# Optimization experiments

Hardware: AMD Instinct MI355X
Metric: run time of the kernel (lower is better)

The kernel has to match this reference:

```python
import jax, jax.numpy as jnp
import numpy as np

BATCH, SEQ, H, P, HID, CHUNK = 2, 2048, 32, 64, 2048, 256
NORM_EPS = 1e-5


def setup_inputs() -> dict:
    key = jax.random.key(0)
    ks = jax.random.split(key, 10)
    f = lambda k, sh, sc=1.0: jax.random.normal(k, sh, jnp.float32) * sc
    return {
        "hidden_states_ab": f(ks[0], (BATCH, SEQ, HID), 0.02),
        "hidden_states_g": f(ks[1], (BATCH, SEQ, HID), 0.02),
        "q_states": f(ks[2], (BATCH, SEQ, H, P)),
        "k_states": f(ks[3], (BATCH, SEQ, H, P)),
        "v_states": f(ks[4], (BATCH, SEQ, H, P)),
        "dt_w": f(ks[5], (HID, H), 0.02),
        "dt_b": jnp.zeros((H,), jnp.float32),
        "g_w": f(ks[6], (HID, H), 0.02),
        "g_b": jnp.zeros((H,), jnp.float32),
        "A_log": jnp.log(jnp.arange(1, H + 1, dtype=jnp.float32)),
        "dt_bias": jnp.ones((H,), jnp.float32),
        "norm_weight": jnp.ones((H * P,), jnp.float32),
        "o_w": f(ks[7], (H, P, P), 0.02),
        "o_b": jnp.zeros((H, P), jnp.float32),
    }


def _l2norm(x, eps=1e-12):
    # torch F.normalize(p=2, dim=-1): x / max(||x||, eps)
    n = jnp.sqrt(jnp.sum(x * x, axis=-1, keepdims=True))
    return x / jnp.maximum(n, eps)


def _ssd(x, dt, A, Bm, Cm, chunk):
    # x: (b,s,h,p)  dt: (b,s,h) post-softplus  A: (h,)  Bm/Cm: (b,s,h,n)
    b, s, h, p = x.shape
    n = Bm.shape[-1]
    c = s // chunk
    rs = lambda t: t.reshape(b, c, chunk, *t.shape[2:])
    x, dt, Bm, Cm = rs(x), rs(dt), rs(Bm), rs(Cm)
    a = dt * A                         # (b,c,L,h) log-decay increments
    cum = jnp.cumsum(a, axis=2)        # (b,c,L,h)
    cumT = jnp.swapaxes(cum, 2, 3)     # (b,c,h,L)
    # intra-chunk (quadratic, causal) part
    diff = cumT[..., :, None] - cumT[..., None, :]          # (b,c,h,L,L)
    mask = jnp.tril(jnp.ones((chunk, chunk), bool))
    decay = jnp.exp(jnp.where(mask, diff, -jnp.inf))
    CB = jnp.einsum('bclhn,bcshn->bchls', Cm, Bm)
    scores = CB * decay * jnp.swapaxes(dt, 2, 3)[:, :, :, None, :]
    y = jnp.einsum('bchls,bcshp->bclhp', scores, x)
    # per-chunk states
    decay_last = jnp.exp(cumT[..., -1:] - cumT)             # (b,c,h,L)
    w = jnp.swapaxes(decay_last, 2, 3) * dt                 # (b,c,L,h)
    states = jnp.einsum('bclh,bclhn,bclhp->bchpn', w, Bm, x)
    # inter-chunk recurrence over c chunks
    chunk_decay = jnp.exp(cumT[..., -1])                    # (b,c,h)
    def step(Hs, inp):
        cd, st = inp
        return cd[..., None, None] * Hs + st, Hs
    H_last, H_prev = jax.lax.scan(
        step, jnp.zeros((b, h, p, n), x.dtype),
        (jnp.moveaxis(chunk_decay, 1, 0), jnp.moveaxis(states, 1, 0)))
    H_prev = jnp.moveaxis(H_prev, 0, 1)                     # (b,c,h,p,n)
    y = y + jnp.einsum('bclhn,bclh,bchpn->bclhp', Cm, jnp.exp(cum), H_prev)
    return y.reshape(b, s, h, p), H_last


def reference(hidden_states_ab, hidden_states_g, q_states, k_states, v_states,
              dt_w, dt_b, g_w, g_b, A_log, dt_bias, norm_weight, o_w, o_b):
    b, s, h, p = v_states.shape
    Cm = _l2norm(q_states)
    Bm = _l2norm(k_states)
    # dt_proj bias + mamba dt_bias, then softplus (dt_softplus=True)
    dt = jax.nn.softplus(hidden_states_ab @ dt_w + dt_b + dt_bias)   # (b,s,h)
    A = -jnp.exp(A_log)
    y, ssm_state = _ssd(v_states, dt, A, Bm, Cm, CHUNK)
    # gate: g_proj then repeat_interleave(head_dim) on last dim
    gate = jnp.repeat(hidden_states_g @ g_w + g_b, p, axis=-1)       # (b,s,h*p)
    # RMSNormGated, norm_before_gate=False: normalize(x * silu(z)) * weight
    y = y.reshape(b, s, h * p) * jax.nn.silu(gate)
    y = y * jax.lax.rsqrt(jnp.mean(y * y, axis=-1, keepdims=True) + NORM_EPS)
    y = y * norm_weight
    # GroupLinear o_proj: per-head (p -> p) linear
    out = jnp.einsum('bshp,hpq->bshq', y.reshape(b, s, h, p), o_w) + o_b
    return out.reshape(b, s, h * p)
```

## Files before the change

kernel.cpp:

```cpp
#include <hip/hip_runtime.h>
#include <math.h>

#define BATCH 2
#define SEQ   2048
#define NH    32
#define HID   2048
#define CHUNK 256
#define NCH   8
#define NBCH  (BATCH*NCH*NH)
#define PST   72
#define BK    256
#define APST  264

typedef __attribute__((ext_vector_type(4))) float f32x4;
typedef __attribute__((ext_vector_type(8))) short bf16x8;
typedef unsigned int uint;
typedef unsigned short ushort;

__device__ __forceinline__ float softplusf(float x) {
    return x > 20.f ? x : log1pf(expf(x));
}

__device__ __forceinline__ short f2bf(float f) {
    union { float f; uint u; } v; v.f = f;
    uint r = v.u + 0x7FFF + ((v.u >> 16) & 1);
    return (short)(r >> 16);
}
__device__ __forceinline__ float bf2f(ushort s) {
    union { uint u; float f; } v; v.u = ((uint)s) << 16; return v.f;
}
__device__ __forceinline__ uint packbf2(float lo, float hi) {
    return (uint)(ushort)f2bf(lo) | ((uint)(ushort)f2bf(hi) << 16);
}

struct BF8 { union { bf16x8 v; short s[8]; }; };

__device__ __forceinline__ bf16x8 load_cvt8(const float* p, float scale) {
    float4 a = *(const float4*)p;
    float4 b = *(const float4*)(p + 4);
    BF8 r;
    r.s[0]=f2bf(a.x*scale); r.s[1]=f2bf(a.y*scale); r.s[2]=f2bf(a.z*scale); r.s[3]=f2bf(a.w*scale);
    r.s[4]=f2bf(b.x*scale); r.s[5]=f2bf(b.y*scale); r.s[6]=f2bf(b.z*scale); r.s[7]=f2bf(b.w*scale);
    return r.v;
}

#define MFMA(a,b,c) __builtin_amdgcn_mfma_f32_16x16x32_bf16((a),(b),(c),0,0,0)

__global__ __launch_bounds__(256) void k_proj(
    const float* __restrict__ hs_ab, const float* __restrict__ hs_g,
    const float* __restrict__ dt_w, const float* __restrict__ dt_b,
    const float* __restrict__ g_w,  const float* __restrict__ g_b,
    const float* __restrict__ dt_bias,
    float* __restrict__ dt_out, float* __restrict__ g_out)
{
    __shared__ short As[32 * APST];
    __shared__ short Bs[32 * APST];
    int which = blockIdx.x & 1;
    int rt = blockIdx.x >> 1;
    int r0 = rt * 32;
    const float* Am = which ? hs_g : hs_ab;
    const float* W  = which ? g_w  : dt_w;
    int t = threadIdx.x;
    int w = t >> 6, lane = t & 63, quad = lane >> 4, l16 = lane & 15;
    int mh = w & 1, nh = w >> 1;

    f32x4 acc = (f32x4){0.f, 0.f, 0.f, 0.f};

    for (int kc = 0; kc < HID; kc += BK) {
        __syncthreads();
        {
            int row = t >> 3, k0 = (t & 7) * 32;
            const float* src = Am + (size_t)(r0 + row) * HID + kc + k0;
            uint* dst = (uint*)(As + row * APST + k0);
            #pragma unroll
            for (int i = 0; i < 4; ++i) {
                float4 a = *(const float4*)(src + i * 8);
                float4 b = *(const float4*)(src + i * 8 + 4);
                dst[i*4+0] = packbf2(a.x, a.y); dst[i*4+1] = packbf2(a.z, a.w);
                dst[i*4+2] = packbf2(b.x, b.y); dst[i*4+3] = packbf2(b.z, b.w);
            }
        }
        if (t < 128) {
            int k2 = t * 2;
            const float* w0 = W + (size_t)(kc + k2) * NH;
            const float* w1 = w0 + NH;
            #pragma unroll
            for (int n = 0; n < 32; n += 4) {
                float4 a = *(const float4*)(w0 + n);
                float4 b = *(const float4*)(w1 + n);
                *((uint*)(Bs + (n+0) * APST + k2)) = packbf2(a.x, b.x);
                *((uint*)(Bs + (n+1) * APST + k2)) = packbf2(a.y, b.y);
                *((uint*)(Bs + (n+2) * APST + k2)) = packbf2(a.z, b.z);
                *((uint*)(Bs + (n+3) * APST + k2)) = packbf2(a.w, b.w);
            }
        }
        __syncthreads();
        #pragma unroll
        for (int ks = 0; ks < BK / 32; ++ks) {
            bf16x8 af = *(const bf16x8*)(As + (mh*16 + l16) * APST + ks*32 + quad*8);
            bf16x8 bf = *(const bf16x8*)(Bs + (nh*16 + l16) * APST + ks*32 + quad*8);
            acc = MFMA(af, bf, acc);
        }
    }

    int n = nh * 16 + l16;
    int Rb = r0 + mh * 16 + quad * 4;
    if (which == 0) {
        float bb = dt_b[n] + dt_bias[n];
        #pragma unroll
        for (int r = 0; r < 4; ++r)
            dt_out[(size_t)(Rb + r) * NH + n] = softplusf(acc[r] + bb);
    } else {
        float bb = g_b[n];
        #pragma unroll
        for (int r = 0; r < 4; ++r)
            g_out[(size_t)(Rb + r) * NH + n] = acc[r] + bb;
    }
}

__global__ __launch_bounds__(256) void k_norms(
    const float* __restrict__ q, const float* __restrict__ k,
    float* __restrict__ invC, float* __restrict__ invB)
{
    int t = threadIdx.x;
    int lane = t & 63;
    size_t row = (size_t)blockIdx.x * 4 + (t >> 6);
    float qv = q[row * 64 + lane];
    float kv = k[row * 64 + lane];
    float sq = qv * qv, sk = kv * kv;
    #pragma unroll
    for (int off = 32; off > 0; off >>= 1) {
        sq += __shfl_down(sq, off);
        sk += __shfl_down(sk, off);
    }
    if (lane == 0) {
        invC[row] = 1.f / fmaxf(sqrtf(sq), 1e-12f);
        invB[row] = 1.f / fmaxf(sqrtf(sk), 1e-12f);
    }
}

__global__ __launch_bounds__(256) void k_cumsum(
    const float* __restrict__ dt, const float* __restrict__ A_log,
    float* __restrict__ cumc, float* __restrict__ wvc,
    float* __restrict__ dtc, float* __restrict__ cd)
{
    __shared__ float sC[256];
    int bch = blockIdx.x;
    int h = bch & 31, c = (bch >> 5) & 7, b = bch >> 8;
    int t = threadIdx.x;
    size_t row = ((size_t)b * SEQ + c * CHUNK + t) * NH + h;
    float dt_l = dt[row];
    float A = -expf(A_log[h]);
    sC[t] = dt_l * A;
    __syncthreads();
    for (int off = 1; off < 256; off <<= 1) {
        float v = (t >= off) ? sC[t - off] : 0.f;
        __syncthreads();
        sC[t] += v;
        __syncthreads();
    }
    float cum = sC[t], cl = sC[255];
    size_t o = (size_t)bch * CHUNK + t;
    cumc[o] = cum;
    wvc[o] = expf(cl - cum) * dt_l;
    dtc[o] = dt_l;
    if (t == 255) cd[bch] = expf(cl);
}

__global__ __launch_bounds__(256) void k_states(
    const float* __restrict__ kst, const float* __restrict__ vst,
    const float* __restrict__ invB, const float* __restrict__ wvc,
    float* __restrict__ sp)
{
    __shared__ float kS[64 * 64];
    __shared__ float xS[64 * 64];
    int blk = blockIdx.x;
    int half = blk & 1, bch = blk >> 1;
    int h = bch & 31, c = (bch >> 5) & 7, b = bch >> 8;
    int t = threadIdx.x;
    size_t rowbase = (size_t)b * SEQ + c * CHUNK + half * 128;
    int pg = (t & 15) * 4, ng = (t >> 4) * 4;
    float acc[4][4];
    #pragma unroll
    for (int i = 0; i < 4; ++i)
        #pragma unroll
        for (int j = 0; j < 4; ++j) acc[i][j] = 0.f;

    for (int tt = 0; tt < 2; ++tt) {
        int r0 = t >> 4;
        int c4 = (t & 15) * 4;
        #pragma unroll
        for (int i = 0; i < 4; ++i) {
            int row = r0 + i * 16;
            size_t grow = (rowbase + tt * 64 + row) * NH + h;
            float w  = wvc[(size_t)bch * CHUNK + half * 128 + tt * 64 + row];
            float ib = invB[grow];
            float4 kv = *(const float4*)(kst + grow * 64 + c4);
            float4 xv = *(const float4*)(vst + grow * 64 + c4);
            *(float4*)(kS + row * 64 + c4) =
                make_float4(kv.x * ib, kv.y * ib, kv.z * ib, kv.w * ib);
            *(float4*)(xS + row * 64 + c4) =
                make_float4(xv.x * w, xv.y * w, xv.z * w, xv.w * w);
        }
        __syncthreads();
        for (int ll = 0; ll < 64; ++ll) {
            float4 x4 = *(const float4*)(xS + ll * 64 + pg);
            float4 k4 = *(const float4*)(kS + ll * 64 + ng);
            acc[0][0] += x4.x * k4.x; acc[0][1] += x4.x * k4.y;
            acc[0][2] += x4.x * k4.z; acc[0][3] += x4.x * k4.w;
            acc[1][0] += x4.y * k4.x; acc[1][1] += x4.y * k4.y;
            acc[1][2] += x4.y * k4.z; acc[1][3] += x4.y * k4.w;
            acc[2][0] += x4.z * k4.x; acc[2][1] += x4.z * k4.y;
            acc[2][2] += x4.z * k4.z; acc[2][3] += x4.z * k4.w;
            acc[3][0] += x4.w * k4.x; acc[3][1] += x4.w * k4.y;
            acc[3][2] += x4.w * k4.z; acc[3][3] += x4.w * k4.w;
        }
        __syncthreads();
    }
    size_t obase = (size_t)blk * 4096;
    #pragma unroll
    for (int i = 0; i < 4; ++i)
        *(float4*)(sp + obase + (pg + i) * 64 + ng) =
            make_float4(acc[i][0], acc[i][1], acc[i][2], acc[i][3]);
}

__global__ __launch_bounds__(256) void k_scan(
    const float* __restrict__ sp, const float* __restrict__ cd,
    float* __restrict__ Hp)
{
    size_t id = (size_t)blockIdx.x * 256 + threadIdx.x;
    size_t bh = id >> 12, pn = id & 4095;
    size_t b = bh >> 5, h = bh & 31;
    float carry = 0.f;
    for (int c = 0; c < NCH; ++c) {
        size_t bch = (b * NCH + c) * NH + h;
        float st = sp[(bch * 2) * 4096 + pn] + sp[(bch * 2 + 1) * 4096 + pn];
        Hp[bch * 4096 + pn] = carry;
        carry = cd[bch] * carry + st;
    }
}

__global__ __launch_bounds__(256, 2) void k_intra(
    const float* __restrict__ qst, const float* __restrict__ kst,
    const float* __restrict__ vst,
    const float* __restrict__ invC, const float* __restrict__ invB,
    const float* __restrict__ cumc, const float* __restrict__ dtc,
    const float* __restrict__ Hp,
    short* __restrict__ ygb)
{
    __shared__ short B_s[64 * PST];
    __shared__ short XT_s[64 * PST];
    __shared__ short P_s[4 * 32 * PST];
    __shared__ float sCum[256];
    __shared__ float sDt[256];

    int bch = blockIdx.x;
    int h = bch & 31, c = (bch >> 5) & 7, b = bch >> 8;
    int t = threadIdx.x;
    int w = t >> 6, lane = t & 63;
    int quad = lane >> 4, l16 = lane & 15;
    size_t rowbase = (size_t)b * SEQ + c * CHUNK;

    sCum[t] = cumc[(size_t)bch * CHUNK + t];
    sDt[t]  = dtc[(size_t)bch * CHUNK + t];
    __syncthreads();

    bf16x8 cf[2][2][2];
    #pragma unroll
    for (int is = 0; is < 2; ++is) {
        int strip = is ? (7 - w) : w;
        #pragma unroll
        for (int lt = 0; lt < 2; ++lt) {
            int l = strip * 32 + lt * 16 + l16;
            size_t grow = (rowbase + l) * NH + h;
            float ic = invC[grow];
            const float* qp = qst + grow * 64 + quad * 8;
            cf[is][lt][0] = load_cvt8(qp, ic);
            cf[is][lt][1] = load_cvt8(qp + 32, ic);
        }
    }

    f32x4 acc[2][2][4];
    #pragma unroll
    for (int is = 0; is < 2; ++is)
        #pragma unroll
        for (int lt = 0; lt < 2; ++lt)
            #pragma unroll
            for (int pt = 0; pt < 4; ++pt)
                acc[is][lt][pt] = (f32x4){0.f, 0.f, 0.f, 0.f};

    {
        bf16x8 hf[4][2];
        #pragma unroll
        for (int pt = 0; pt < 4; ++pt) {
            const float* hp = Hp + (size_t)bch * 4096 + (pt * 16 + l16) * 64 + quad * 8;
            hf[pt][0] = load_cvt8(hp, 1.f);
            hf[pt][1] = load_cvt8(hp + 32, 1.f);
        }
        #pragma unroll
        for (int is = 0; is < 2; ++is)
            #pragma unroll
            for (int lt = 0; lt < 2; ++lt)
                #pragma unroll
                for (int pt = 0; pt < 4; ++pt) {
                    acc[is][lt][pt] = MFMA(cf[is][lt][0], hf[pt][0], acc[is][lt][pt]);
                    acc[is][lt][pt] = MFMA(cf[is][lt][1], hf[pt][1], acc[is][lt][pt]);
                }
    }
    #pragma unroll
    for (int is = 0; is < 2; ++is) {
        int strip = is ? (7 - w) : w;
        #pragma unroll
        for (int lt = 0; lt < 2; ++lt) {
            float e[4];
            #pragma unroll
            for (int r = 0; r < 4; ++r)
                e[r] = __expf(sCum[strip * 32 + lt * 16 + quad * 4 + r]);
            #pragma unroll
            for (int pt = 0; pt < 4; ++pt)
                #pragma unroll
                for (int r = 0; r < 4; ++r)
                    acc[is][lt][pt][r] *= e[r];
        }
    }

    short* Pw = P_s + w * 32 * PST;

    for (int st = 0; st < 4; ++st) {
        __syncthreads();
        {
            int ss = t >> 2, q4 = (t & 3) * 16;
            size_t grow = (rowbase + st * 64 + ss) * NH + h;
            float ib = invB[grow];
            const float4* kp = (const float4*)(kst + grow * 64 + q4);
            float4 v0 = kp[0], v1 = kp[1], v2 = kp[2], v3 = kp[3];
            uint u[8];
            u[0] = packbf2(v0.x * ib, v0.y * ib); u[1] = packbf2(v0.z * ib, v0.w * ib);
            u[2] = packbf2(v1.x * ib, v1.y * ib); u[3] = packbf2(v1.z * ib, v1.w * ib);
            u[4] = packbf2(v2.x * ib, v2.y * ib); u[5] = packbf2(v2.z * ib, v2.w * ib);
            u[6] = packbf2(v3.x * ib, v3.y * ib); u[7] = packbf2(v3.z * ib, v3.w * ib);
            uint* dst = (uint*)(B_s + ss * PST + q4);
            *(uint4*)dst = make_uint4(u[0], u[1], u[2], u[3]);
            *(uint4*)(dst + 4) = make_uint4(u[4], u[5], u[6], u[7]);
        }
        {
            int ss2 = t & 31, qh = t >> 5;
            int p0 = qh * 8;
            size_t g0 = (rowbase + st * 64 + 2 * ss2) * NH + h;
            size_t g1 = g0 + NH;
            float dt0 = sDt[st * 64 + 2 * ss2];
            float dt1 = sDt[st * 64 + 2 * ss2 + 1];
            float4 a0 = *(const float4*)(vst + g0 * 64 + p0);
            float4 a1 = *(const float4*)(vst + g0 * 64 + p0 + 4);
            float4 b0 = *(const float4*)(vst + g1 * 64 + p0);
            float4 b1 = *(const float4*)(vst + g1 * 64 + p0 + 4);
            float x0[8] = {a0.x, a0.y, a0.z, a0.w, a1.x, a1.y, a1.z, a1.w};
            float x1[8] = {b0.x, b0.y, b0.z, b0.w, b1.x, b1.y, b1.z, b1.w};
            uint* xt = (uint*)XT_s;
            #pragma unroll
            for (int i = 0; i < 8; ++i)
                xt[(p0 + i) * (PST / 2) + ss2] = packbf2(x0[i] * dt0, x1[i] * dt1);
        }
        __syncthreads();

        bf16x8 xf[4][2];
        #pragma unroll
        for (int pt = 0; pt < 4; ++pt) {
            #pragma unroll
            for (int ks = 0; ks < 2; ++ks)
                xf[pt][ks] = *(const bf16x8*)(XT_s + (pt * 16 + l16) * PST + ks * 32 + quad * 8);
        }

        #pragma unroll
        for (int is = 0; is < 2; ++is) {
            int strip = is ? (7 - w) : w;
            int L0 = strip * 32;
            if (L0 + 31 < st * 64) continue;

            #pragma unroll
            for (int lt = 0; lt < 2; ++lt) {
                int Lt = L0 + lt * 16;
                float cl = sCum[Lt + l16];
                int lrow = lt * 16 + l16;
                #pragma unroll
                for (int mt = 0; mt < 4; ++mt) {
                    int S0 = st * 64 + mt * 16;
                    uint* pdst = (uint*)(Pw + lrow * PST + mt * 16 + quad * 4);
                    if (S0 > Lt + 15) {
                        *(uint2*)pdst = make_uint2(0u, 0u);
                        continue;
                    }
                    f32x4 sa = (f32x4){0.f, 0.f, 0.f, 0.f};
                    bf16x8 af0 = *(const bf16x8*)(B_s + (mt * 16 + l16) * PST + quad * 8);
                    bf16x8 af1 = *(const bf16x8*)(B_s + (mt * 16 + l16) * PST + 32 + quad * 8);
                    sa = MFMA(af0, cf[is][lt][0], sa);
                    sa = MFMA(af1, cf[is][lt][1], sa);
                    float vals[4];
                    #pragma unroll
                    for (int r = 0; r < 4; ++r) {
                        int s = S0 + quad * 4 + r;
                        float v = sa[r] * __expf(cl - sCum[s]);
                        vals[r] = (Lt + l16 >= s) ? v : 0.f;
                    }
                    *(uint2*)pdst = make_uint2(packbf2(vals[0], vals[1]),
                                               packbf2(vals[2], vals[3]));
                }
            }
            #pragma unroll
            for (int lt = 0; lt < 2; ++lt) {
                int Lmax = L0 + lt * 16 + 15;
                #pragma unroll
                for (int ks = 0; ks < 2; ++ks) {
                    if (st * 64 + ks * 32 > Lmax) continue;
                    bf16x8 af = *(const bf16x8*)(Pw + (lt * 16 + l16) * PST + ks * 32 + quad * 8);
                    #pragma unroll
                    for (int pt = 0; pt < 4; ++pt)
                        acc[is][lt][pt] = MFMA(af, xf[pt][ks], acc[is][lt][pt]);
                }
            }
        }
    }

    #pragma unroll
    for (int is = 0; is < 2; ++is) {
        int strip = is ? (7 - w) : w;
        #pragma unroll
        for (int lt = 0; lt < 2; ++lt)
            #pragma unroll
            for (int pt = 0; pt < 4; ++pt)
                #pragma unroll
                for (int r = 0; r < 4; ++r) {
                    int l = strip * 32 + lt * 16 + quad * 4 + r;
                    int p = pt * 16 + l16;
                    ygb[((rowbase + l) * NH + h) * 64 + p] = f2bf(acc[is][lt][pt][r]);
                }
    }
}

__global__ __launch_bounds__(256) void k_gate(
    const short* __restrict__ ygb, const float* __restrict__ g_ws,
    const float* __restrict__ norm_w, short* __restrict__ ygn)
{
    __shared__ float sil[32];
    __shared__ float red[256];
    int r = blockIdx.x;
    int t = threadIdx.x;
    if (t < 32) {
        float g = g_ws[(size_t)r * 32 + t];
        sil[t] = g / (1.f + expf(-g));
    }
    __syncthreads();
    uint4 u = *(const uint4*)(ygb + (size_t)r * 2048 + t * 8);
    float s = sil[t >> 3];
    float v[8];
    v[0] = bf2f(u.x & 0xFFFF) * s; v[1] = bf2f(u.x >> 16) * s;
    v[2] = bf2f(u.y & 0xFFFF) * s; v[3] = bf2f(u.y >> 16) * s;
    v[4] = bf2f(u.z & 0xFFFF) * s; v[5] = bf2f(u.z >> 16) * s;
    v[6] = bf2f(u.w & 0xFFFF) * s; v[7] = bf2f(u.w >> 16) * s;
    float ssq = 0.f;
    #pragma unroll
    for (int i = 0; i < 8; ++i) ssq += v[i] * v[i];
    red[t] = ssq;
    __syncthreads();
    for (int off = 128; off > 0; off >>= 1) {
        if (t < off) red[t] += red[t + off];
        __syncthreads();
    }
    float scale = rsqrtf(red[0] / 2048.f + 1e-5f);
    const float* nw = norm_w + t * 8;
    uint4 o;
    o.x = packbf2(v[0] * scale * nw[0], v[1] * scale * nw[1]);
    o.y = packbf2(v[2] * scale * nw[2], v[3] * scale * nw[3]);
    o.z = packbf2(v[4] * scale * nw[4], v[5] * scale * nw[5]);
    o.w = packbf2(v[6] * scale * nw[6], v[7] * scale * nw[7]);
    *(uint4*)(ygn + (size_t)r * 2048 + t * 8) = o;
}

__global__ __launch_bounds__(256) void k_oproj(
    const short* __restrict__ ygn, const float* __restrict__ o_w,
    const float* __restrict__ o_b, float* __restrict__ out)
{
    __shared__ short wT[64 * PST];
    int blk = blockIdx.x;
    int h = blk & 31, rt = blk >> 5;
    int t = threadIdx.x;
    int w = t >> 6, lane = t & 63;
    int quad = lane >> 4, l16 = lane & 15;

    {
        int p = t >> 2, q4 = (t & 3) * 16;
        const float* wp = o_w + (size_t)h * 4096 + p * 64 + q4;
        float4 v0 = *(const float4*)wp, v1 = *(const float4*)(wp + 4);
        float4 v2 = *(const float4*)(wp + 8), v3 = *(const float4*)(wp + 12);
        float vv[16] = {v0.x,v0.y,v0.z,v0.w, v1.x,v1.y,v1.z,v1.w,
                        v2.x,v2.y,v2.z,v2.w, v3.x,v3.y,v3.z,v3.w};
        #pragma unroll
        for (int i = 0; i < 16; ++i)
            wT[(q4 + i) * PST + p] = f2bf(vv[i]);
    }
    __syncthreads();

    bf16x8 bfr[4][2];
    #pragma unroll
    for (int nt = 0; nt < 4; ++nt)
        #pragma unroll
        for (int ks = 0; ks < 2; ++ks)
            bfr[nt][ks] = *(const bf16x8*)(wT + (nt * 16 + l16) * PST + ks * 32 + quad * 8);

    int rowbase = rt * 256 + w * 64;
    f32x4 acc[4][4];
    #pragma unroll
    for (int nt = 0; nt < 4; ++nt) {
        float bv = o_b[h * 64 + nt * 16 + l16];
        #pragma unroll
        for (int mt = 0; mt < 4; ++mt)
            acc[mt][nt] = (f32x4){bv, bv, bv, bv};
    }
    #pragma unroll
    for (int ks = 0; ks < 2; ++ks) {
        #pragma unroll
        for (int mt = 0; mt < 4; ++mt) {
            int row = rowbase + mt * 16 + l16;
            bf16x8 af = *(const bf16x8*)(ygn + (size_t)row * 2048 + h * 64 + ks * 32 + quad * 8);
            #pragma unroll
            for (int nt = 0; nt < 4; ++nt)
                acc[mt][nt] = MFMA(af, bfr[nt][ks], acc[mt][nt]);
        }
    }
    #pragma unroll
    for (int mt = 0; mt < 4; ++mt)
        #pragma unroll
        for (int nt = 0; nt < 4; ++nt)
            #pragma unroll
            for (int r = 0; r < 4; ++r) {
                int row = rowbase + mt * 16 + quad * 4 + r;
                out[(size_t)row * 2048 + h * 64 + nt * 16 + l16] = acc[mt][nt][r];
            }
}

extern "C" void kernel_launch(void* const* d_in, const int* in_sizes, int n_in,
                              void* d_out, int out_size, void* d_ws, size_t ws_size,
                              hipStream_t stream) {
    const float* hs_ab   = (const float*)d_in[0];
    const float* hs_g    = (const float*)d_in[1];
    const float* qst     = (const float*)d_in[2];
    const float* kst     = (const float*)d_in[3];
    const float* vst     = (const float*)d_in[4];
    const float* dt_w    = (const float*)d_in[5];
    const float* dt_b    = (const float*)d_in[6];
    const float* g_w     = (const float*)d_in[7];
    const float* g_b     = (const float*)d_in[8];
    const float* A_log   = (const float*)d_in[9];
    const float* dt_bias = (const float*)d_in[10];
    const float* norm_w  = (const float*)d_in[11];
    const float* o_w     = (const float*)d_in[12];
    const float* o_b     = (const float*)d_in[13];
    float* out = (float*)d_out;

    float* ws = (float*)d_ws;
    size_t off = 0;
    float* dt_ws  = ws + off; off += (size_t)BATCH * SEQ * NH;
    float* g_ws   = ws + off; off += (size_t)BATCH * SEQ * NH;
    float* invC   = ws + off; off += (size_t)BATCH * SEQ * NH;
    float* invB   = ws + off; off += (size_t)BATCH * SEQ * NH;
    float* cumc   = ws + off; off += (size_t)NBCH * CHUNK;
    float* wvc    = ws + off; off += (size_t)NBCH * CHUNK;
    float* dtc    = ws + off; off += (size_t)NBCH * CHUNK;
    float* cd_ws  = ws + off; off += (size_t)NBCH;
    float* sp     = ws + off; off += (size_t)NBCH * 2 * 4096;
    float* Hp     = ws + off; off += (size_t)NBCH * 4096;

    short* ygb = (short*)sp;
    short* ygn = (short*)sp + (size_t)BATCH * SEQ * NH * 64;

    k_proj<<<2 * (BATCH * SEQ / 32), 256, 0, stream>>>(hs_ab, hs_g, dt_w, dt_b,
                                                       g_w, g_b, dt_bias, dt_ws, g_ws);
    k_norms<<<BATCH * SEQ * NH / 4, 256, 0, stream>>>(qst, kst, invC, invB);
    k_cumsum<<<NBCH, 256, 0, stream>>>(dt_ws, A_log, cumc, wvc, dtc, cd_ws);
    k_states<<<NBCH * 2, 256, 0, stream>>>(kst, vst, invB, wvc, sp);
    k_scan<<<BATCH * NH * 4096 / 256, 256, 0, stream>>>(sp, cd_ws, Hp);
    k_intra<<<NBCH, 256, 0, stream>>>(qst, kst, vst, invC, invB,
                                      cumc, dtc, Hp, ygb);
    k_gate<<<BATCH * SEQ, 256, 0, stream>>>(ygb, g_ws, norm_w, ygn);
    k_oproj<<<32 * (BATCH * SEQ / 256), 256, 0, stream>>>(ygn, o_w, o_b, out);
}
```

Before: 288.2 us.

## Split-K the dt/gate projection GEMM with a separate reduction kernel

The projection kernel previously launched 256 blocks, each looping over the full 2048-wide K dimension. It now splits K into four segments, launching 1024 blocks that write partial sums to a workspace. A new finalize kernel adds the partials, applies the biases, and applies softplus for dt. This is meant to fill the GPU's compute units better on a skinny GEMM, at the cost of an extra launch and extra global traffic for the partial sums.

```diff
diff --git a/kernel.cpp b/kernel.cpp
--- a/kernel.cpp
+++ b/kernel.cpp
@@ -11,6 +11,8 @@
 #define PST   72
 #define BK    256
 #define APST  264
+#define KSPLIT 4
+#define KSEG  (HID / KSPLIT)
 
 typedef __attribute__((ext_vector_type(4))) float f32x4;
 typedef __attribute__((ext_vector_type(8))) short bf16x8;
@@ -48,15 +50,16 @@
 
 __global__ __launch_bounds__(256) void k_proj(
     const float* __restrict__ hs_ab, const float* __restrict__ hs_g,
-    const float* __restrict__ dt_w, const float* __restrict__ dt_b,
-    const float* __restrict__ g_w,  const float* __restrict__ g_b,
-    const float* __restrict__ dt_bias,
-    float* __restrict__ dt_out, float* __restrict__ g_out)
+    const float* __restrict__ dt_w, const float* __restrict__ g_w,
+    float* __restrict__ part)
 {
     __shared__ short As[32 * APST];
     __shared__ short Bs[32 * APST];
-    int which = blockIdx.x & 1;
-    int rt = blockIdx.x >> 1;
+    int blk = blockIdx.x;
+    int ksp = blk >> 8;
+    int rem = blk & 255;
+    int which = rem >> 7;
+    int rt = rem & 127;
     int r0 = rt * 32;
     const float* Am = which ? hs_g : hs_ab;
     const float* W  = which ? g_w  : dt_w;
@@ -66,7 +69,7 @@
 
     f32x4 acc = (f32x4){0.f, 0.f, 0.f, 0.f};
 
-    for (int kc = 0; kc < HID; kc += BK) {
+    for (int kc = ksp * KSEG; kc < ksp * KSEG + KSEG; kc += BK) {
         __syncthreads();
         {
             int row = t >> 3, k0 = (t & 7) * 32;
@@ -105,17 +108,28 @@
 
     int n = nh * 16 + l16;
     int Rb = r0 + mh * 16 + quad * 4;
-    if (which == 0) {
-        float bb = dt_b[n] + dt_bias[n];
-        #pragma unroll
-        for (int r = 0; r < 4; ++r)
-            dt_out[(size_t)(Rb + r) * NH + n] = softplusf(acc[r] + bb);
-    } else {
-        float bb = g_b[n];
-        #pragma unroll
-        for (int r = 0; r < 4; ++r)
-            g_out[(size_t)(Rb + r) * NH + n] = acc[r] + bb;
-    }
+    float* pd = part + ((size_t)(which * KSPLIT + ksp) * 4096 + Rb) * 32 + n;
+    #pragma unroll
+    for (int r = 0; r < 4; ++r)
+        pd[r * 32] = acc[r];
+}
+
+__global__ __launch_bounds__(256) void k_proj_fin(
+    const float* __restrict__ part,
+    const float* __restrict__ dt_b, const float* __restrict__ g_b,
+    const float* __restrict__ dt_bias,
+    float* __restrict__ dt_out, float* __restrict__ g_out)
+{
+    int id = blockIdx.x * 256 + threadIdx.x;
+    int which = id >> 17;
+    int rid = id & 131071;
+    int n = rid & 31;
+    const float* p = part + (size_t)which * (KSPLIT * 131072) + rid;
+    float s = p[0] + p[131072] + p[262144] + p[393216];
+    if (which == 0)
+        dt_out[rid] = softplusf(s + dt_b[n] + dt_bias[n]);
+    else
+        g_out[rid] = s + g_b[n];
 }
 
 __global__ __launch_bounds__(256) void k_norms(
@@ -559,6 +573,7 @@
 
     float* ws = (float*)d_ws;
     size_t off = 0;
+    float* part   = ws + off; off += (size_t)2 * KSPLIT * 4096 * 32;
     float* dt_ws  = ws + off; off += (size_t)BATCH * SEQ * NH;
     float* g_ws   = ws + off; off += (size_t)BATCH * SEQ * NH;
     float* invC   = ws + off; off += (size_t)BATCH * SEQ * NH;
@@ -573,8 +588,10 @@
     short* ygb = (short*)sp;
     short* ygn = (short*)sp + (size_t)BATCH * SEQ * NH * 64;
 
-    k_proj<<<2 * (BATCH * SEQ / 32), 256, 0, stream>>>(hs_ab, hs_g, dt_w, dt_b,
-                                                       g_w, g_b, dt_bias, dt_ws, g_ws);
+    k_proj<<<2 * KSPLIT * (BATCH * SEQ / 32), 256, 0, stream>>>(
+        hs_ab, hs_g, dt_w, g_w, part);
+    k_proj_fin<<<2 * BATCH * SEQ * NH / 256, 256, 0, stream>>>(
+        part, dt_b, g_b, dt_bias, dt_ws, g_ws);
     k_norms<<<BATCH * SEQ * NH / 4, 256, 0, stream>>>(qst, kst, invC, invB);
     k_cumsum<<<NBCH, 256, 0, stream>>>(dt_ws, A_log, cumc, wvc, dtc, cd_ws);
     k_states<<<NBCH * 2, 256, 0, stream>>>(kst, vst, invB, wvc, sp);
```

Result: no change. 286.7 us (-0.5%).
